# Optimization experiments

Measured on AMD Instinct MI355X. Metric: run time of the kernel, lower is better.

Reference implementation:

```python
import jax, jax.numpy as jnp
import numpy as np

NPOINT, RADIUS, NSAMPLE = 1024, 0.2, 32
EPS = 1e-5


def _fps(xyz, npoint):
    # Iterative farthest point sampling (deterministic start at index 0).
    B, N, _ = xyz.shape
    def step(carry, _):
        distance, farthest = carry
        centroid = jnp.take_along_axis(xyz, farthest[:, None, None], axis=1)  # (B,1,3)
        d = jnp.sum((xyz - centroid) ** 2, -1)                                # (B,N)
        distance = jnp.minimum(distance, d)
        return (distance, jnp.argmax(distance, -1)), farthest
    init = (jnp.full((B, N), 1e10, xyz.dtype), jnp.zeros((B,), jnp.int32))
    _, idx = jax.lax.scan(step, init, None, length=npoint)
    return idx.T  # (B, npoint)


def _gather(points, idx):
    # points (B,N,C), idx (B,S,K) -> (B,S,K,C)
    B, S, K = idx.shape
    flat = jnp.take_along_axis(points, idx.reshape(B, S * K)[:, :, None], axis=1)
    return flat.reshape(B, S, K, points.shape[-1])


def _query_ball(xyz, new_xyz):
    # For each centroid, first NSAMPLE point indices within RADIUS (pad with first hit).
    B, N, _ = xyz.shape
    sqr = jnp.sum((new_xyz[:, :, None, :] - xyz[:, None, :, :]) ** 2, -1)  # (B,S,N)
    gi = jnp.where(sqr > RADIUS ** 2, N, jnp.arange(N, dtype=jnp.int32)[None, None, :])
    gi = jnp.sort(gi, axis=-1)[:, :, :NSAMPLE]
    return jnp.where(gi == N, gi[:, :, :1], gi)  # (B,S,K)


def _cond_layer(x, t_embed, wt, bt, wc, bc, g, b):
    # ConditionalConv1d: x += time_mlp(gelu(t)); 1x1 conv; BatchNorm (batch stats); GELU.
    tp = jax.nn.gelu(t_embed, approximate=False) @ wt.T + bt      # (B,Cin)
    x = x + tp[:, None, None, :]
    y = jnp.einsum('bskc,oc->bsko', x, wc) + bc                   # (B,S,K,Cout)
    mu = jnp.mean(y, axis=(0, 1, 2))
    var = jnp.var(y, axis=(0, 1, 2))
    y = (y - mu) * jax.lax.rsqrt(var + EPS) * g + b
    return jax.nn.gelu(y, approximate=False)


def _forward(xyz, points, t_embed, params):
    fps_idx = _fps(xyz, NPOINT)                                        # (B,S)
    new_xyz = jnp.take_along_axis(xyz, fps_idx[:, :, None], axis=1)    # (B,S,3)
    idx = _query_ball(xyz, new_xyz)                                    # (B,S,K)
    grouped_xyz = _gather(xyz, idx) - new_xyz[:, :, None, :]           # (B,S,K,3)
    grouped_pts = _gather(jnp.swapaxes(points, 1, 2), idx)             # (B,S,K,C)
    x = jnp.concatenate([grouped_xyz, grouped_pts], -1)                # (B,S,K,C+3)
    for p in params:
        x = _cond_layer(x, t_embed, *p)
    new_points = jnp.swapaxes(jnp.max(x, axis=2), 1, 2)                # (B,Cout,S)
    return new_xyz, new_points


def setup_inputs() -> dict:
    key = jax.random.key(0)
    ks = iter(jax.random.split(key, 32))
    B, N, CIN, T = 8, 4096, 64, 128
    chans = [(CIN + 3, 64), (64, 64), (64, 128)]
    inp = {
        "xyz": jax.random.normal(next(ks), (B, N, 3), jnp.float32),
        "points": jax.random.normal(next(ks), (B, CIN, N), jnp.float32),
        "t_embed": jax.random.normal(next(ks), (B, T), jnp.float32),
    }
    for i, (ci, co) in enumerate(chans):
        inp[f"wt{i}"] = jax.random.normal(next(ks), (ci, T), jnp.float32) * 0.05
        inp[f"bt{i}"] = jnp.zeros((ci,), jnp.float32)
        inp[f"wc{i}"] = jax.random.normal(next(ks), (co, ci), jnp.float32) * 0.1
        inp[f"bc{i}"] = jnp.zeros((co,), jnp.float32)
        inp[f"g{i}"] = jnp.ones((co,), jnp.float32)
        inp[f"be{i}"] = jnp.zeros((co,), jnp.float32)
    return inp


def reference(xyz, points, t_embed,
              wt0, bt0, wc0, bc0, g0, be0,
              wt1, bt1, wc1, bc1, g1, be1,
              wt2, bt2, wc2, bc2, g2, be2):
    params = [(wt0, bt0, wc0, bc0, g0, be0),
              (wt1, bt1, wc1, bc1, g1, be1),
              (wt2, bt2, wc2, bc2, g2, be2)]
    return _forward(xyz, points, t_embed, params)
```

## Files before the change

kernel.cpp:

```cpp
#include <hip/hip_runtime.h>
#include <cmath>

#define Bc 8
#define Nc 4096
#define Sc 1024
#define Kc 32
#define Mc (Bc*Sc*Kc)

typedef float v2f __attribute__((ext_vector_type(2)));

__device__ __forceinline__ float gelu_f(float x){
  return 0.5f*x*(1.0f + erff(x*0.70710678f));
}

__device__ __forceinline__ v2f pk_add(v2f a, v2f b){
  v2f d; asm("v_pk_add_f32 %0, %1, %2" : "=v"(d) : "v"(a), "v"(b)); return d;
}
__device__ __forceinline__ v2f pk_mul(v2f a, v2f b){
  v2f d; asm("v_pk_mul_f32 %0, %1, %2" : "=v"(d) : "v"(a), "v"(b)); return d;
}

#define ROR_MAXF(v, n) { int _t = __builtin_amdgcn_update_dpp(__float_as_int(v), __float_as_int(v), 0x120|(n), 0xF, 0xF, false); \
                         v = fmaxf(v, __int_as_float(_t)); }
#define BC15_MAXF(v)   { int _t = __builtin_amdgcn_update_dpp(__float_as_int(v), __float_as_int(v), 0x142, 0xA, 0xF, false); \
                         v = fmaxf(v, __int_as_float(_t)); }
#define BC31_MAXF(v)   { int _t = __builtin_amdgcn_update_dpp(__float_as_int(v), __float_as_int(v), 0x143, 0xC, 0xF, false); \
                         v = fmaxf(v, __int_as_float(_t)); }

#define TK(v_, i_) { const bool _t = ((v_) > Bv) || (((v_) == Bv) && ((i_) < Bi)); \
  Bv = _t ? (v_) : Bv; Bi = _t ? (i_) : Bi; }

__global__ __launch_bounds__(256) void fused_front_kernel(
    const float* __restrict__ xyz, float* __restrict__ new_xyz,
    const float* __restrict__ points, float* __restrict__ pointsT,
    const float* __restrict__ t_embed,
    const float* __restrict__ wt0, const float* __restrict__ bt0,
    const float* __restrict__ wt1, const float* __restrict__ bt1,
    const float* __restrict__ wt2, const float* __restrict__ bt2,
    float* __restrict__ tp)
{
  __shared__ __align__(16) float smem[17424];
  const int bid = blockIdx.x;
  const int tid = threadIdx.x;

  if (bid < 8){
    const int b = bid;
    const int lane = tid & 63;
    const int wv = tid >> 6;
    const float* xb = xyz + b*Nc*3;
    float*    skv   = smem;
    unsigned* ski   = (unsigned*)(smem + 8);
    int*      shist = (int*)(smem + 16);
    float4*   c4    = (float4*)(smem + 1040);

    const int base = tid << 4;
    float4 f[12];
    const float4* src = (const float4*)(xb + base*3);
#pragma unroll
    for (int q=0;q<12;++q) f[q] = src[q];
#define AR(i) ((i)%4==0 ? f[(i)/4].x : (i)%4==1 ? f[(i)/4].y : (i)%4==2 ? f[(i)/4].z : f[(i)/4].w)
    v2f px2[8], py2[8], pz2[8], d2[8];
#pragma unroll
    for (int k=0;k<8;++k){
      px2[k].x = AR(6*k+0); py2[k].x = AR(6*k+1); pz2[k].x = AR(6*k+2);
      px2[k].y = AR(6*k+3); py2[k].y = AR(6*k+4); pz2[k].y = AR(6*k+5);
      c4[base+2*k  ] = make_float4(px2[k].x, py2[k].x, pz2[k].x, 0.f);
      c4[base+2*k+1] = make_float4(px2[k].y, py2[k].y, pz2[k].y, 0.f);
      d2[k].x = 1e10f; d2[k].y = 1e10f;
    }
#undef AR
    __syncthreads();
    int widx = 0;
    for (int it=0; it<Sc; ++it){
      const float4 cc = c4[widx];
      if (tid==0) shist[it] = widx;
      v2f ncx, ncy, ncz;
      ncx.x=-cc.x; ncx.y=-cc.x; ncy.x=-cc.y; ncy.y=-cc.y; ncz.x=-cc.z; ncz.y=-cc.z;
      float bvx=-1.0f, bvy=-1.0f;
#pragma unroll
      for (int k=0;k<8;++k){
        const v2f dx = pk_add(px2[k], ncx);
        const v2f dy = pk_add(py2[k], ncy);
        const v2f dz = pk_add(pz2[k], ncz);
        const v2f dd = pk_add(pk_add(pk_mul(dx,dx), pk_mul(dy,dy)), pk_mul(dz,dz));
        v2f dn;
        dn.x = fminf(d2[k].x, dd.x);
        dn.y = fminf(d2[k].y, dd.y);
        d2[k] = dn;
        bvx = fmaxf(bvx, dn.x);
        bvy = fmaxf(bvy, dn.y);
      }
      const float bv = fmaxf(bvx, bvy);
      unsigned bi_local = 0xFFFFFFFFu;
#pragma unroll
      for (int k=0;k<8;++k){
        const unsigned c0 = (d2[k].x == bv) ? (unsigned)(base + 2*k    ) : 0xFFFFFFFFu;
        const unsigned c1 = (d2[k].y == bv) ? (unsigned)(base + 2*k + 1) : 0xFFFFFFFFu;
        const unsigned cm = (c0 < c1) ? c0 : c1;
        bi_local = (cm < bi_local) ? cm : bi_local;
      }
      float mv = bv;
      ROR_MAXF(mv,1); ROR_MAXF(mv,2); ROR_MAXF(mv,4); ROR_MAXF(mv,8);
      BC15_MAXF(mv); BC31_MAXF(mv);
      mv = __int_as_float(__builtin_amdgcn_readlane(__float_as_int(mv), 63));
      const unsigned long long mk = __ballot(bv == mv);
      const int src_lane = __ffsll(mk) - 1;
      const unsigned bi = (unsigned)__builtin_amdgcn_readlane((int)bi_local, src_lane);
      const int p4 = (it & 1) << 2;
      if (lane==0){ skv[p4+wv] = mv; ski[p4+wv] = bi; }
      __syncthreads();
      const float4 m4 = *reinterpret_cast<const float4*>(&skv[p4]);
      const uint4  i4 = *reinterpret_cast<const uint4*>(&ski[p4]);
      float Bv = m4.x; unsigned Bi = i4.x;
      TK(m4.y, i4.y) TK(m4.z, i4.z) TK(m4.w, i4.w)
      widx = (int)Bi;
    }
    __syncthreads();
    for (int i = tid; i < Sc; i += 256){
      const float4 cc = c4[shist[i]];
      float* o = new_xyz + ((size_t)b*Sc + i)*3;
      o[0]=cc.x; o[1]=cc.y; o[2]=cc.z;
    }
  } else if (bid < 520){
    const int t  = bid - 8;
    const int tb = t >> 6;
    const int n0 = (t & 63) << 6;
    float (*tile)[65] = (float(*)[65])smem;
    const int sub = tid >> 6;
    const int ln  = tid & 63;
#pragma unroll 4
    for (int cp=0; cp<16; ++cp){
      const int c = (cp<<2) + sub;
      tile[c][ln] = points[((size_t)(tb*64+c))*Nc + n0 + ln];
    }
    __syncthreads();
#pragma unroll 4
    for (int np=0; np<16; ++np){
      const int nl = (np<<2) + sub;
      pointsT[((size_t)(tb*Nc + n0 + nl))*64 + ln] = tile[ln][nl];
    }
  } else {
    float* ge = smem;
    for (int i = tid; i < Bc*128; i += 256) ge[i] = gelu_f(t_embed[i]);
    __syncthreads();
    for (int i = tid; i < 3*Bc*68; i += 256){
      const int l = i / (Bc*68);
      const int r = i - l*(Bc*68);
      const int b = r / 68;
      const int c = r - b*68;
      const int ci = (l==0) ? 67 : 64;
      float v = 0.0f;
      if (c < ci){
        const float* wt = (l==0)?wt0:((l==1)?wt1:wt2);
        const float* bt = (l==0)?bt0:((l==1)?bt1:bt2);
        const float* w = wt + c*128;
        const float* g = ge + b*128;
        float acc = 0.0f;
        for (int t2=0;t2<128;++t2) acc = fmaf(g[t2], w[t2], acc);
        v = acc + bt[c];
      }
      tp[i] = v;
    }
  }
}

__global__ __launch_bounds__(256) void ball_kernel(const float* __restrict__ xyz,
    const float* __restrict__ new_xyz, int* __restrict__ ballidx){
  const int g = (blockIdx.x<<2) + (threadIdx.x>>6);
  const int lane = threadIdx.x & 63;
  const int w = threadIdx.x >> 6;
  const int b = g >> 10;
  const float* xb = xyz + b*Nc*3;
  const float cx = new_xyz[g*3+0];
  const float cy = new_xyz[g*3+1];
  const float cz = new_xyz[g*3+2];
  __shared__ int sidx[4][32];
  int total = 0;
  for (int base=0; base<Nc; base+=64){
    const int i = base + lane;
    float dx=__fsub_rn(cx, xb[i*3+0]);
    float dy=__fsub_rn(cy, xb[i*3+1]);
    float dz=__fsub_rn(cz, xb[i*3+2]);
    float sq=__fadd_rn(__fadd_rn(__fmul_rn(dx,dx),__fmul_rn(dy,dy)),__fmul_rn(dz,dz));
    bool hit = !(sq > 0.04f);
    unsigned long long m = __ballot(hit);
    if (hit){
      int pos = total + (int)__popcll(m & ((1ull<<lane)-1ull));
      if (pos < 32) sidx[w][pos] = i;
    }
    total += (int)__popcll(m);
    if (total >= 32) break;
  }
  __syncthreads();
  const int fill = (total < 32) ? total : 32;
  const int first = sidx[w][0];
  if (lane >= fill && lane < 32) sidx[w][lane] = first;
  if (lane < 32) ballidx[(g<<5)+lane] = sidx[w][lane];
}

__global__ __launch_bounds__(256) void gather_kernel(const float* __restrict__ xyz,
    const float* __restrict__ new_xyz, const float* __restrict__ pointsT,
    const int* __restrict__ ballidx, float* __restrict__ X){
  const int bs = blockIdx.x;
  const int b = bs >> 10;
  const int w = threadIdx.x >> 6;
  const int lane = threadIdx.x & 63;
  const float cx=new_xyz[bs*3+0], cy=new_xyz[bs*3+1], cz=new_xyz[bs*3+2];
  for (int k=w; k<32; k+=4){
    const int pidx = ballidx[(bs<<5)+k];
    const float* pt = pointsT + ((size_t)((b<<12)+pidx))*64;
    const float* xp = xyz + ((size_t)((b<<12)+pidx))*3;
    float* xr = X + (size_t)((bs<<5)+k)*68;
    float v;
    if      (lane==0) v = __fsub_rn(xp[0], cx);
    else if (lane==1) v = __fsub_rn(xp[1], cy);
    else if (lane==2) v = __fsub_rn(xp[2], cz);
    else              v = pt[lane-3];
    xr[lane] = v;
    if (lane < 4){
      int c = 64 + lane;
      xr[c] = (c<67) ? pt[c-3] : 0.0f;
    }
  }
}

template<int NORMIN, int CI_REAL, int CI_PAD, int LDX>
__global__ __launch_bounds__(256) void mm_kernel(const float* X,
    const float* __restrict__ wc, const float* __restrict__ tp,
    const float* __restrict__ sc_in, const float* __restrict__ sh_in,
    float* Y, float* __restrict__ pS, float* __restrict__ pQ, int o_base)
{
  __shared__ __align__(16) float wT[CI_PAD][64];
  __shared__ __align__(16) float tpr[CI_PAD];
  __shared__ __align__(16) float scN[64], shN[64];
  __shared__ float redS[4][64];
  __shared__ float redQ[4][64];
  const int tid = threadIdx.x;
  const int m0 = blockIdx.x << 8;
  const int b  = blockIdx.x >> 7;
  for (int idx = tid; idx < CI_PAD*64; idx += 256){
    int c = idx >> 6, o = idx & 63;
    wT[c][o] = (c < CI_REAL) ? wc[(o_base + o)*CI_REAL + c] : 0.0f;
  }
  if (tid < CI_PAD) tpr[tid] = tp[b*68 + tid];
  if (NORMIN && tid < 64){ scN[tid] = sc_in[tid]; shN[tid] = sh_in[tid]; }
  __syncthreads();
  const int rg = tid >> 2, cg = tid & 3;
  const float* x0 = X + (size_t)(m0 + (rg<<2)) * LDX;
  float4 acc[4][4];
#pragma unroll
  for (int r=0;r<4;++r)
#pragma unroll
    for (int q=0;q<4;++q) acc[r][q] = make_float4(0.f,0.f,0.f,0.f);

  for (int c = 0; c < CI_PAD; c += 4){
    const float4 tpv = *reinterpret_cast<const float4*>(&tpr[c]);
    float4 sci, shi;
    if (NORMIN){
      sci = *reinterpret_cast<const float4*>(&scN[c]);
      shi = *reinterpret_cast<const float4*>(&shN[c]);
    }
    float4 xr[4];
#pragma unroll
    for (int r=0;r<4;++r){
      float4 xv = *reinterpret_cast<const float4*>(x0 + r*LDX + c);
      if (NORMIN){
        xv.x = gelu_f(fmaf(xv.x, sci.x, shi.x));
        xv.y = gelu_f(fmaf(xv.y, sci.y, shi.y));
        xv.z = gelu_f(fmaf(xv.z, sci.z, shi.z));
        xv.w = gelu_f(fmaf(xv.w, sci.w, shi.w));
      }
      xr[r] = make_float4(xv.x+tpv.x, xv.y+tpv.y, xv.z+tpv.z, xv.w+tpv.w);
    }
#pragma unroll
    for (int cc=0; cc<4; ++cc){
      const float* wrow = &wT[c+cc][cg<<4];
      const float4 w0 = *reinterpret_cast<const float4*>(wrow);
      const float4 w1 = *reinterpret_cast<const float4*>(wrow+4);
      const float4 w2 = *reinterpret_cast<const float4*>(wrow+8);
      const float4 w3 = *reinterpret_cast<const float4*>(wrow+12);
#pragma unroll
      for (int r=0;r<4;++r){
        const float xs = (cc==0)?xr[r].x:((cc==1)?xr[r].y:((cc==2)?xr[r].z:xr[r].w));
        acc[r][0].x = fmaf(xs, w0.x, acc[r][0].x);
        acc[r][0].y = fmaf(xs, w0.y, acc[r][0].y);
        acc[r][0].z = fmaf(xs, w0.z, acc[r][0].z);
        acc[r][0].w = fmaf(xs, w0.w, acc[r][0].w);
        acc[r][1].x = fmaf(xs, w1.x, acc[r][1].x);
        acc[r][1].y = fmaf(xs, w1.y, acc[r][1].y);
        acc[r][1].z = fmaf(xs, w1.z, acc[r][1].z);
        acc[r][1].w = fmaf(xs, w1.w, acc[r][1].w);
        acc[r][2].x = fmaf(xs, w2.x, acc[r][2].x);
        acc[r][2].y = fmaf(xs, w2.y, acc[r][2].y);
        acc[r][2].z = fmaf(xs, w2.z, acc[r][2].z);
        acc[r][2].w = fmaf(xs, w2.w, acc[r][2].w);
        acc[r][3].x = fmaf(xs, w3.x, acc[r][3].x);
        acc[r][3].y = fmaf(xs, w3.y, acc[r][3].y);
        acc[r][3].z = fmaf(xs, w3.z, acc[r][3].z);
        acc[r][3].w = fmaf(xs, w3.w, acc[r][3].w);
      }
    }
  }
#pragma unroll
  for (int r=0;r<4;++r){
    float4* yp = reinterpret_cast<float4*>(Y + (size_t)(m0 + (rg<<2) + r)*64 + (cg<<4));
#pragma unroll
    for (int q=0;q<4;++q) yp[q] = acc[r][q];
  }
  float4 s[4], q2[4];
#pragma unroll
  for (int q=0;q<4;++q){
    float sx=0,sy=0,sz=0,sw=0, qx=0,qy=0,qz=0,qw=0;
#pragma unroll
    for (int r=0;r<4;++r){
      sx+=acc[r][q].x; qx+=acc[r][q].x*acc[r][q].x;
      sy+=acc[r][q].y; qy+=acc[r][q].y*acc[r][q].y;
      sz+=acc[r][q].z; qz+=acc[r][q].z*acc[r][q].z;
      sw+=acc[r][q].w; qw+=acc[r][q].w*acc[r][q].w;
    }
    s[q]=make_float4(sx,sy,sz,sw); q2[q]=make_float4(qx,qy,qz,qw);
  }
  const int lane = tid & 63, wvv = tid >> 6;
#pragma unroll
  for (int off=32; off>=4; off>>=1){
#pragma unroll
    for (int q=0;q<4;++q){
      s[q].x  += __shfl_down(s[q].x,  off);
      s[q].y  += __shfl_down(s[q].y,  off);
      s[q].z  += __shfl_down(s[q].z,  off);
      s[q].w  += __shfl_down(s[q].w,  off);
      q2[q].x += __shfl_down(q2[q].x, off);
      q2[q].y += __shfl_down(q2[q].y, off);
      q2[q].z += __shfl_down(q2[q].z, off);
      q2[q].w += __shfl_down(q2[q].w, off);
    }
  }
  if (lane < 4){
#pragma unroll
    for (int q=0;q<4;++q){
      redS[wvv][lane*16 + q*4 + 0] = s[q].x;
      redS[wvv][lane*16 + q*4 + 1] = s[q].y;
      redS[wvv][lane*16 + q*4 + 2] = s[q].z;
      redS[wvv][lane*16 + q*4 + 3] = s[q].w;
      redQ[wvv][lane*16 + q*4 + 0] = q2[q].x;
      redQ[wvv][lane*16 + q*4 + 1] = q2[q].y;
      redQ[wvv][lane*16 + q*4 + 2] = q2[q].z;
      redQ[wvv][lane*16 + q*4 + 3] = q2[q].w;
    }
  }
  __syncthreads();
  if (tid < 64){
    float a=0.f, bb=0.f;
#pragma unroll
    for (int w2=0; w2<4; ++w2){ a += redS[w2][tid]; bb += redQ[w2][tid]; }
    pS[(blockIdx.x<<6) + tid] = a;
    pQ[(blockIdx.x<<6) + tid] = bb;
  }
}

__global__ __launch_bounds__(256) void finalize_kernel(const float* __restrict__ pS,
    const float* __restrict__ pQ, const float* __restrict__ g, const float* __restrict__ be,
    float* __restrict__ scale, float* __restrict__ shift, int nblk){
  __shared__ float rS[4][64], rQ[4][64];
  const int o = threadIdx.x & 63;
  const int ch = threadIdx.x >> 6;
  const int per = nblk >> 2;
  float s=0.f, q=0.f;
  const int i0 = ch*per;
#pragma unroll 4
  for (int i=0;i<per;++i){
    s += pS[((i0+i)<<6)+o];
    q += pQ[((i0+i)<<6)+o];
  }
  rS[ch][o]=s; rQ[ch][o]=q;
  __syncthreads();
  if (threadIdx.x < 64){
    float ss = rS[0][o]+rS[1][o]+rS[2][o]+rS[3][o];
    float qq = rQ[0][o]+rQ[1][o]+rQ[2][o]+rQ[3][o];
    const float inv_n = 1.0f/(float)Mc;
    const float mu = ss*inv_n;
    const float var = qq*inv_n - mu*mu;
    const float rs = 1.0f/sqrtf(var + 1e-5f);
    const float sc = rs*g[o];
    scale[o] = sc;
    shift[o] = fmaf(-mu, sc, be[o]);
  }
}

__global__ __launch_bounds__(256) void pool_kernel(const float* __restrict__ Y,
    const float* __restrict__ scale, const float* __restrict__ shift,
    float* __restrict__ out, int o_base){
  __shared__ float pool[32][65];
  const int tid = threadIdx.x;
  const int b  = blockIdx.x >> 5;
  const int s0 = (blockIdx.x & 31) << 5;
  const int c  = tid & 63;
  const int sl0 = tid >> 6;
  const float sc = scale[c], sh = shift[c];
  for (int sp=0; sp<8; ++sp){
    const int sl = (sp<<2) + sl0;
    const int s = s0 + sl;
    const float* yp = Y + ((size_t)((b<<10)+s)<<5)*64 + c;
    float mx = -1e30f;
#pragma unroll 4
    for (int k=0;k<32;++k){
      float v = yp[(size_t)(k<<6)];
      v = gelu_f(fmaf(v, sc, sh));
      mx = fmaxf(mx, v);
    }
    pool[sl][c] = mx;
  }
  __syncthreads();
  for (int p=0;p<8;++p){
    const int c2 = (p<<3) + (tid>>5);
    const int sl = tid & 31;
    out[((size_t)((b<<7) + o_base + c2)<<10) + s0 + sl] = pool[sl][c2];
  }
}

extern "C" void kernel_launch(void* const* d_in, const int* in_sizes, int n_in,
                              void* d_out, int out_size, void* d_ws, size_t ws_size,
                              hipStream_t stream){
  const float* xyz     = (const float*)d_in[0];
  const float* points  = (const float*)d_in[1];
  const float* t_embed = (const float*)d_in[2];
  const float* wt0=(const float*)d_in[3],  *bt0=(const float*)d_in[4],  *wc0=(const float*)d_in[5];
  const float* g0 =(const float*)d_in[7],  *be0=(const float*)d_in[8];
  const float* wt1=(const float*)d_in[9],  *bt1=(const float*)d_in[10], *wc1=(const float*)d_in[11];
  const float* g1 =(const float*)d_in[13], *be1=(const float*)d_in[14];
  const float* wt2=(const float*)d_in[15], *bt2=(const float*)d_in[16], *wc2=(const float*)d_in[17];
  const float* g2 =(const float*)d_in[19], *be2=(const float*)d_in[20];

  float* out_xyz = (float*)d_out;
  float* out_pts = (float*)d_out + Bc*Sc*3;

  float* ws       = (float*)d_ws;
  float* tp       = ws + 0;
  float* pointsT  = ws + 2048;
  int*   ballidx  = (int*)(ws + 2099200);
  float* X        = ws + 2361344;
  float* Ya       = ws + 20187136;
  float* pS0      = ws + 36964352;
  float* pQ0      = ws + 37029888;
  float* pS1      = ws + 37095424;
  float* pQ1      = ws + 37160960;
  float* sc0      = ws + 37226496;
  float* sh0      = sc0 + 64;
  float* sc1      = sc0 + 128;
  float* sh1      = sc0 + 192;
  float* sc2      = sc0 + 256;
  float* sh2      = sc0 + 320;
  float* sc3      = sc0 + 384;
  float* sh3      = sc0 + 448;
  float* Yx       = X;

  fused_front_kernel<<<521, 256, 0, stream>>>(xyz, out_xyz, points, pointsT,
      t_embed, wt0,bt0, wt1,bt1, wt2,bt2, tp);
  ball_kernel<<<(Bc*Sc)/4, 256, 0, stream>>>(xyz, out_xyz, ballidx);
  gather_kernel<<<Bc*Sc, 256, 0, stream>>>(xyz, out_xyz, pointsT, ballidx, X);

  mm_kernel<0,67,68,68><<<Mc/256, 256, 0, stream>>>(X, wc0, tp, nullptr, nullptr, Ya, pS0, pQ0, 0);
  finalize_kernel<<<1, 256, 0, stream>>>(pS0, pQ0, g0, be0, sc0, sh0, Mc/256);

  mm_kernel<1,64,64,64><<<Mc/256, 256, 0, stream>>>(Ya, wc1, tp + 544, sc0, sh0, Ya, pS0, pQ0, 0);
  finalize_kernel<<<1, 256, 0, stream>>>(pS0, pQ0, g1, be1, sc1, sh1, Mc/256);

  mm_kernel<1,64,64,64><<<Mc/256, 256, 0, stream>>>(Ya, wc2, tp + 1088, sc1, sh1, Yx, pS0, pQ0, 0);
  mm_kernel<1,64,64,64><<<Mc/256, 256, 0, stream>>>(Ya, wc2, tp + 1088, sc1, sh1, Ya, pS1, pQ1, 64);
  finalize_kernel<<<1, 256, 0, stream>>>(pS0, pQ0, g2,    be2,    sc2, sh2, Mc/256);
  finalize_kernel<<<1, 256, 0, stream>>>(pS1, pQ1, g2+64, be2+64, sc3, sh3, Mc/256);

  pool_kernel<<<Bc*Sc/32, 256, 0, stream>>>(Yx, sc2, sh2, out_pts, 0);
  pool_kernel<<<Bc*Sc/32, 256, 0, stream>>>(Ya, sc3, sh3, out_pts, 64);
}
```

Measured before the change: 1.323 ms.

## Carry FPS centroid coords in registers and fuse ball query with gather

The FPS loop no longer stages all points in shared memory and looks up the selected centroid by index. Each lane now keeps the coordinates of its local argmax, broadcasts them via readlane, and reduces them through shared memory together with the value and index. Thread 0 writes new_xyz directly each iteration, replacing the final history pass. The ball query and gather kernels are merged so the 32 neighbor indices stay in shared memory instead of a global ballidx round trip. This saves a launch, but each wave now gathers its own 32 rows serially, and a __syncthreads was dropped in favour of wave-local shared memory access.

```diff
diff --git a/kernel.cpp b/kernel.cpp
--- a/kernel.cpp
+++ b/kernel.cpp
@@ -27,8 +27,8 @@
 #define BC31_MAXF(v)   { int _t = __builtin_amdgcn_update_dpp(__float_as_int(v), __float_as_int(v), 0x143, 0xC, 0xF, false); \
                          v = fmaxf(v, __int_as_float(_t)); }
 
-#define TK(v_, i_) { const bool _t = ((v_) > Bv) || (((v_) == Bv) && ((i_) < Bi)); \
-  Bv = _t ? (v_) : Bv; Bi = _t ? (i_) : Bi; }
+#define TK5(kk, i_) { const bool _t = ((kk).x > Bv) || (((kk).x == Bv) && ((i_) < Bi)); \
+  Bv=_t?(kk).x:Bv; Bi=_t?(i_):Bi; Bx=_t?(kk).y:Bx; By=_t?(kk).z:By; Bz=_t?(kk).w:Bz; }
 
 __global__ __launch_bounds__(256) void fused_front_kernel(
     const float* __restrict__ xyz, float* __restrict__ new_xyz,
@@ -39,7 +39,7 @@
     const float* __restrict__ wt2, const float* __restrict__ bt2,
     float* __restrict__ tp)
 {
-  __shared__ __align__(16) float smem[17424];
+  __shared__ __align__(16) float smem[4160];
   const int bid = blockIdx.x;
   const int tid = threadIdx.x;
 
@@ -48,10 +48,8 @@
     const int lane = tid & 63;
     const int wv = tid >> 6;
     const float* xb = xyz + b*Nc*3;
-    float*    skv   = smem;
-    unsigned* ski   = (unsigned*)(smem + 8);
-    int*      shist = (int*)(smem + 16);
-    float4*   c4    = (float4*)(smem + 1040);
+    float4*   skc = (float4*)smem;
+    unsigned* ski = (unsigned*)(smem + 32);
 
     const int base = tid << 4;
     float4 f[12];
@@ -64,18 +62,17 @@
     for (int k=0;k<8;++k){
       px2[k].x = AR(6*k+0); py2[k].x = AR(6*k+1); pz2[k].x = AR(6*k+2);
       px2[k].y = AR(6*k+3); py2[k].y = AR(6*k+4); pz2[k].y = AR(6*k+5);
-      c4[base+2*k  ] = make_float4(px2[k].x, py2[k].x, pz2[k].x, 0.f);
-      c4[base+2*k+1] = make_float4(px2[k].y, py2[k].y, pz2[k].y, 0.f);
       d2[k].x = 1e10f; d2[k].y = 1e10f;
     }
 #undef AR
-    __syncthreads();
-    int widx = 0;
+    float cx = xb[0], cy = xb[1], cz = xb[2];
     for (int it=0; it<Sc; ++it){
-      const float4 cc = c4[widx];
-      if (tid==0) shist[it] = widx;
+      if (tid==0){
+        float* o = new_xyz + ((size_t)b*Sc + it)*3;
+        o[0]=cx; o[1]=cy; o[2]=cz;
+      }
       v2f ncx, ncy, ncz;
-      ncx.x=-cc.x; ncx.y=-cc.x; ncy.x=-cc.y; ncy.y=-cc.y; ncz.x=-cc.z; ncz.y=-cc.z;
+      ncx.x=-cx; ncx.y=-cx; ncy.x=-cy; ncy.y=-cy; ncz.x=-cz; ncz.y=-cz;
       float bvx=-1.0f, bvy=-1.0f;
 #pragma unroll
       for (int k=0;k<8;++k){
@@ -91,35 +88,37 @@
         bvy = fmaxf(bvy, dn.y);
       }
       const float bv = fmaxf(bvx, bvy);
-      unsigned bi_local = 0xFFFFFFFFu;
+      unsigned bi = 0xFFFFFFFFu; float bx=0.f, by=0.f, bz=0.f;
 #pragma unroll
       for (int k=0;k<8;++k){
-        const unsigned c0 = (d2[k].x == bv) ? (unsigned)(base + 2*k    ) : 0xFFFFFFFFu;
-        const unsigned c1 = (d2[k].y == bv) ? (unsigned)(base + 2*k + 1) : 0xFFFFFFFFu;
-        const unsigned cm = (c0 < c1) ? c0 : c1;
-        bi_local = (cm < bi_local) ? cm : bi_local;
+        if ((d2[k].x == bv) && (bi == 0xFFFFFFFFu)){
+          bi = (unsigned)(base + 2*k); bx = px2[k].x; by = py2[k].x; bz = pz2[k].x;
+        }
+        if ((d2[k].y == bv) && (bi == 0xFFFFFFFFu)){
+          bi = (unsigned)(base + 2*k + 1); bx = px2[k].y; by = py2[k].y; bz = pz2[k].y;
+        }
       }
       float mv = bv;
       ROR_MAXF(mv,1); ROR_MAXF(mv,2); ROR_MAXF(mv,4); ROR_MAXF(mv,8);
       BC15_MAXF(mv); BC31_MAXF(mv);
       mv = __int_as_float(__builtin_amdgcn_readlane(__float_as_int(mv), 63));
       const unsigned long long mk = __ballot(bv == mv);
-      const int src_lane = __ffsll(mk) - 1;
-      const unsigned bi = (unsigned)__builtin_amdgcn_readlane((int)bi_local, src_lane);
+      const int sl = __ffsll(mk) - 1;
+      const unsigned wbi = (unsigned)__builtin_amdgcn_readlane((int)bi, sl);
+      const float wbx = __int_as_float(__builtin_amdgcn_readlane(__float_as_int(bx), sl));
+      const float wby = __int_as_float(__builtin_amdgcn_readlane(__float_as_int(by), sl));
+      const float wbz = __int_as_float(__builtin_amdgcn_readlane(__float_as_int(bz), sl));
       const int p4 = (it & 1) << 2;
-      if (lane==0){ skv[p4+wv] = mv; ski[p4+wv] = bi; }
+      if (lane==0){ skc[p4+wv] = make_float4(mv, wbx, wby, wbz); ski[p4+wv] = wbi; }
       __syncthreads();
-      const float4 m4 = *reinterpret_cast<const float4*>(&skv[p4]);
-      const uint4  i4 = *reinterpret_cast<const uint4*>(&ski[p4]);
-      float Bv = m4.x; unsigned Bi = i4.x;
-      TK(m4.y, i4.y) TK(m4.z, i4.z) TK(m4.w, i4.w)
-      widx = (int)Bi;
-    }
-    __syncthreads();
-    for (int i = tid; i < Sc; i += 256){
-      const float4 cc = c4[shist[i]];
-      float* o = new_xyz + ((size_t)b*Sc + i)*3;
-      o[0]=cc.x; o[1]=cc.y; o[2]=cc.z;
+      const float4 k0 = skc[p4+0];
+      const float4 k1 = skc[p4+1];
+      const float4 k2 = skc[p4+2];
+      const float4 k3 = skc[p4+3];
+      const uint4  ii = *reinterpret_cast<const uint4*>(&ski[p4]);
+      float Bv = k0.x; unsigned Bi = ii.x; float Bx = k0.y, By = k0.z, Bz = k0.w;
+      TK5(k1, ii.y) TK5(k2, ii.z) TK5(k3, ii.w)
+      cx = Bx; cy = By; cz = Bz;
     }
   } else if (bid < 520){
     const int t  = bid - 8;
@@ -164,8 +163,9 @@
   }
 }
 
-__global__ __launch_bounds__(256) void ball_kernel(const float* __restrict__ xyz,
-    const float* __restrict__ new_xyz, int* __restrict__ ballidx){
+__global__ __launch_bounds__(256) void ballgather_kernel(const float* __restrict__ xyz,
+    const float* __restrict__ new_xyz, const float* __restrict__ pointsT,
+    float* __restrict__ X){
   const int g = (blockIdx.x<<2) + (threadIdx.x>>6);
   const int lane = threadIdx.x & 63;
   const int w = threadIdx.x >> 6;
@@ -191,34 +191,21 @@
     total += (int)__popcll(m);
     if (total >= 32) break;
   }
-  __syncthreads();
   const int fill = (total < 32) ? total : 32;
   const int first = sidx[w][0];
   if (lane >= fill && lane < 32) sidx[w][lane] = first;
-  if (lane < 32) ballidx[(g<<5)+lane] = sidx[w][lane];
-}
-
-__global__ __launch_bounds__(256) void gather_kernel(const float* __restrict__ xyz,
-    const float* __restrict__ new_xyz, const float* __restrict__ pointsT,
-    const int* __restrict__ ballidx, float* __restrict__ X){
-  const int bs = blockIdx.x;
-  const int b = bs >> 10;
-  const int w = threadIdx.x >> 6;
-  const int lane = threadIdx.x & 63;
-  const float cx=new_xyz[bs*3+0], cy=new_xyz[bs*3+1], cz=new_xyz[bs*3+2];
-  for (int k=w; k<32; k+=4){
-    const int pidx = ballidx[(bs<<5)+k];
+  for (int k=0; k<32; ++k){
+    const int pidx = sidx[w][k];
     const float* pt = pointsT + ((size_t)((b<<12)+pidx))*64;
-    const float* xp = xyz + ((size_t)((b<<12)+pidx))*3;
-    float* xr = X + (size_t)((bs<<5)+k)*68;
+    float* xr = X + (size_t)((g<<5)+k)*68;
     float v;
-    if      (lane==0) v = __fsub_rn(xp[0], cx);
-    else if (lane==1) v = __fsub_rn(xp[1], cy);
-    else if (lane==2) v = __fsub_rn(xp[2], cz);
+    if      (lane==0) v = __fsub_rn(xb[pidx*3+0], cx);
+    else if (lane==1) v = __fsub_rn(xb[pidx*3+1], cy);
+    else if (lane==2) v = __fsub_rn(xb[pidx*3+2], cz);
     else              v = pt[lane-3];
     xr[lane] = v;
     if (lane < 4){
-      int c = 64 + lane;
+      const int c = 64 + lane;
       xr[c] = (c<67) ? pt[c-3] : 0.0f;
     }
   }
@@ -437,7 +424,6 @@
   float* ws       = (float*)d_ws;
   float* tp       = ws + 0;
   float* pointsT  = ws + 2048;
-  int*   ballidx  = (int*)(ws + 2099200);
   float* X        = ws + 2361344;
   float* Ya       = ws + 20187136;
   float* pS0      = ws + 36964352;
@@ -456,8 +442,7 @@
 
   fused_front_kernel<<<521, 256, 0, stream>>>(xyz, out_xyz, points, pointsT,
       t_embed, wt0,bt0, wt1,bt1, wt2,bt2, tp);
-  ball_kernel<<<(Bc*Sc)/4, 256, 0, stream>>>(xyz, out_xyz, ballidx);
-  gather_kernel<<<Bc*Sc, 256, 0, stream>>>(xyz, out_xyz, pointsT, ballidx, X);
+  ballgather_kernel<<<(Bc*Sc)/4, 256, 0, stream>>>(xyz, out_xyz, pointsT, X);
 
   mm_kernel<0,67,68,68><<<Mc/256, 256, 0, stream>>>(X, wc0, tp, nullptr, nullptr, Ya, pS0, pQ0, 0);
   finalize_kernel<<<1, 256, 0, stream>>>(pS0, pQ0, g0, be0, sc0, sh0, Mc/256);
```

Result: slower. 1.594 ms (+20.5%).

## Fuse ball query with gather and halve rows per thread in conv matmul

Applied to the files above, without the earlier changes.

The ball-query and gather kernels are merged, so each wave writes grouped xyz and point features straight from its shared-memory neighbour list. This drops the ballidx global round trip, one kernel launch and a block barrier. The 1x1-conv matmul kernel now computes 2 rows per thread instead of 4, with a register prefetch of the next input chunk, which doubles the number of blocks and lowers register pressure. The per-block partial-statistics buffers are moved and enlarged to hold the doubled block count. In exchange, each wave now gathers its 32 neighbours one after another, and each matmul block loads its weight tile for half as many rows.

```diff
diff --git a/kernel.cpp b/kernel.cpp
--- a/kernel.cpp
+++ b/kernel.cpp
@@ -164,8 +164,9 @@
   }
 }
 
-__global__ __launch_bounds__(256) void ball_kernel(const float* __restrict__ xyz,
-    const float* __restrict__ new_xyz, int* __restrict__ ballidx){
+__global__ __launch_bounds__(256) void ballgather_kernel(const float* __restrict__ xyz,
+    const float* __restrict__ new_xyz, const float* __restrict__ pointsT,
+    float* __restrict__ X){
   const int g = (blockIdx.x<<2) + (threadIdx.x>>6);
   const int lane = threadIdx.x & 63;
   const int w = threadIdx.x >> 6;
@@ -191,34 +192,21 @@
     total += (int)__popcll(m);
     if (total >= 32) break;
   }
-  __syncthreads();
   const int fill = (total < 32) ? total : 32;
   const int first = sidx[w][0];
   if (lane >= fill && lane < 32) sidx[w][lane] = first;
-  if (lane < 32) ballidx[(g<<5)+lane] = sidx[w][lane];
-}
-
-__global__ __launch_bounds__(256) void gather_kernel(const float* __restrict__ xyz,
-    const float* __restrict__ new_xyz, const float* __restrict__ pointsT,
-    const int* __restrict__ ballidx, float* __restrict__ X){
-  const int bs = blockIdx.x;
-  const int b = bs >> 10;
-  const int w = threadIdx.x >> 6;
-  const int lane = threadIdx.x & 63;
-  const float cx=new_xyz[bs*3+0], cy=new_xyz[bs*3+1], cz=new_xyz[bs*3+2];
-  for (int k=w; k<32; k+=4){
-    const int pidx = ballidx[(bs<<5)+k];
+  for (int k=0; k<32; ++k){
+    const int pidx = sidx[w][k];
     const float* pt = pointsT + ((size_t)((b<<12)+pidx))*64;
-    const float* xp = xyz + ((size_t)((b<<12)+pidx))*3;
-    float* xr = X + (size_t)((bs<<5)+k)*68;
+    float* xr = X + (size_t)((g<<5)+k)*68;
     float v;
-    if      (lane==0) v = __fsub_rn(xp[0], cx);
-    else if (lane==1) v = __fsub_rn(xp[1], cy);
-    else if (lane==2) v = __fsub_rn(xp[2], cz);
+    if      (lane==0) v = __fsub_rn(xb[pidx*3+0], cx);
+    else if (lane==1) v = __fsub_rn(xb[pidx*3+1], cy);
+    else if (lane==2) v = __fsub_rn(xb[pidx*3+2], cz);
     else              v = pt[lane-3];
     xr[lane] = v;
     if (lane < 4){
-      int c = 64 + lane;
+      const int c = 64 + lane;
       xr[c] = (c<67) ? pt[c-3] : 0.0f;
     }
   }
@@ -236,8 +224,8 @@
   __shared__ float redS[4][64];
   __shared__ float redQ[4][64];
   const int tid = threadIdx.x;
-  const int m0 = blockIdx.x << 8;
-  const int b  = blockIdx.x >> 7;
+  const int m0 = blockIdx.x << 7;
+  const int b  = blockIdx.x >> 8;
   for (int idx = tid; idx < CI_PAD*64; idx += 256){
     int c = idx >> 6, o = idx & 63;
     wT[c][o] = (c < CI_REAL) ? wc[(o_base + o)*CI_REAL + c] : 0.0f;
@@ -246,32 +234,38 @@
   if (NORMIN && tid < 64){ scN[tid] = sc_in[tid]; shN[tid] = sh_in[tid]; }
   __syncthreads();
   const int rg = tid >> 2, cg = tid & 3;
-  const float* x0 = X + (size_t)(m0 + (rg<<2)) * LDX;
-  float4 acc[4][4];
-#pragma unroll
-  for (int r=0;r<4;++r)
+  const float* x0 = X + (size_t)(m0 + (rg<<1)) * LDX;
+  float4 acc[2][4];
+#pragma unroll
+  for (int r=0;r<2;++r)
 #pragma unroll
     for (int q=0;q<4;++q) acc[r][q] = make_float4(0.f,0.f,0.f,0.f);
 
+  float4 xpf0 = *reinterpret_cast<const float4*>(x0);
+  float4 xpf1 = *reinterpret_cast<const float4*>(x0 + LDX);
+#pragma unroll
   for (int c = 0; c < CI_PAD; c += 4){
+    float4 xc0 = xpf0, xc1 = xpf1;
+    if (c + 4 < CI_PAD){
+      xpf0 = *reinterpret_cast<const float4*>(x0 + (c+4));
+      xpf1 = *reinterpret_cast<const float4*>(x0 + LDX + (c+4));
+    }
     const float4 tpv = *reinterpret_cast<const float4*>(&tpr[c]);
-    float4 sci, shi;
     if (NORMIN){
-      sci = *reinterpret_cast<const float4*>(&scN[c]);
-      shi = *reinterpret_cast<const float4*>(&shN[c]);
-    }
-    float4 xr[4];
-#pragma unroll
-    for (int r=0;r<4;++r){
-      float4 xv = *reinterpret_cast<const float4*>(x0 + r*LDX + c);
-      if (NORMIN){
-        xv.x = gelu_f(fmaf(xv.x, sci.x, shi.x));
-        xv.y = gelu_f(fmaf(xv.y, sci.y, shi.y));
-        xv.z = gelu_f(fmaf(xv.z, sci.z, shi.z));
-        xv.w = gelu_f(fmaf(xv.w, sci.w, shi.w));
-      }
-      xr[r] = make_float4(xv.x+tpv.x, xv.y+tpv.y, xv.z+tpv.z, xv.w+tpv.w);
-    }
+      const float4 sci = *reinterpret_cast<const float4*>(&scN[c]);
+      const float4 shi = *reinterpret_cast<const float4*>(&shN[c]);
+      xc0.x = gelu_f(fmaf(xc0.x, sci.x, shi.x));
+      xc0.y = gelu_f(fmaf(xc0.y, sci.y, shi.y));
+      xc0.z = gelu_f(fmaf(xc0.z, sci.z, shi.z));
+      xc0.w = gelu_f(fmaf(xc0.w, sci.w, shi.w));
+      xc1.x = gelu_f(fmaf(xc1.x, sci.x, shi.x));
+      xc1.y = gelu_f(fmaf(xc1.y, sci.y, shi.y));
+      xc1.z = gelu_f(fmaf(xc1.z, sci.z, shi.z));
+      xc1.w = gelu_f(fmaf(xc1.w, sci.w, shi.w));
+    }
+    float4 xr[2];
+    xr[0] = make_float4(xc0.x+tpv.x, xc0.y+tpv.y, xc0.z+tpv.z, xc0.w+tpv.w);
+    xr[1] = make_float4(xc1.x+tpv.x, xc1.y+tpv.y, xc1.z+tpv.z, xc1.w+tpv.w);
 #pragma unroll
     for (int cc=0; cc<4; ++cc){
       const float* wrow = &wT[c+cc][cg<<4];
@@ -280,7 +274,7 @@
       const float4 w2 = *reinterpret_cast<const float4*>(wrow+8);
       const float4 w3 = *reinterpret_cast<const float4*>(wrow+12);
 #pragma unroll
-      for (int r=0;r<4;++r){
+      for (int r=0;r<2;++r){
         const float xs = (cc==0)?xr[r].x:((cc==1)?xr[r].y:((cc==2)?xr[r].z:xr[r].w));
         acc[r][0].x = fmaf(xs, w0.x, acc[r][0].x);
         acc[r][0].y = fmaf(xs, w0.y, acc[r][0].y);
@@ -302,23 +296,20 @@
     }
   }
 #pragma unroll
-  for (int r=0;r<4;++r){
-    float4* yp = reinterpret_cast<float4*>(Y + (size_t)(m0 + (rg<<2) + r)*64 + (cg<<4));
+  for (int r=0;r<2;++r){
+    float4* yp = reinterpret_cast<float4*>(Y + (size_t)(m0 + (rg<<1) + r)*64 + (cg<<4));
 #pragma unroll
     for (int q=0;q<4;++q) yp[q] = acc[r][q];
   }
   float4 s[4], q2[4];
 #pragma unroll
   for (int q=0;q<4;++q){
-    float sx=0,sy=0,sz=0,sw=0, qx=0,qy=0,qz=0,qw=0;
-#pragma unroll
-    for (int r=0;r<4;++r){
-      sx+=acc[r][q].x; qx+=acc[r][q].x*acc[r][q].x;
-      sy+=acc[r][q].y; qy+=acc[r][q].y*acc[r][q].y;
-      sz+=acc[r][q].z; qz+=acc[r][q].z*acc[r][q].z;
-      sw+=acc[r][q].w; qw+=acc[r][q].w*acc[r][q].w;
-    }
-    s[q]=make_float4(sx,sy,sz,sw); q2[q]=make_float4(qx,qy,qz,qw);
+    s[q]  = make_float4(acc[0][q].x+acc[1][q].x, acc[0][q].y+acc[1][q].y,
+                        acc[0][q].z+acc[1][q].z, acc[0][q].w+acc[1][q].w);
+    q2[q] = make_float4(acc[0][q].x*acc[0][q].x + acc[1][q].x*acc[1][q].x,
+                        acc[0][q].y*acc[0][q].y + acc[1][q].y*acc[1][q].y,
+                        acc[0][q].z*acc[0][q].z + acc[1][q].z*acc[1][q].z,
+                        acc[0][q].w*acc[0][q].w + acc[1][q].w*acc[1][q].w);
   }
   const int lane = tid & 63, wvv = tid >> 6;
 #pragma unroll
@@ -437,13 +428,12 @@
   float* ws       = (float*)d_ws;
   float* tp       = ws + 0;
   float* pointsT  = ws + 2048;
-  int*   ballidx  = (int*)(ws + 2099200);
+  float* pS1      = ws + 2099200;
+  float* pQ1      = ws + 2230272;
   float* X        = ws + 2361344;
   float* Ya       = ws + 20187136;
   float* pS0      = ws + 36964352;
-  float* pQ0      = ws + 37029888;
-  float* pS1      = ws + 37095424;
-  float* pQ1      = ws + 37160960;
+  float* pQ0      = ws + 37095424;
   float* sc0      = ws + 37226496;
   float* sh0      = sc0 + 64;
   float* sc1      = sc0 + 128;
@@ -454,21 +444,22 @@
   float* sh3      = sc0 + 448;
   float* Yx       = X;
 
+  const int NBLK = Mc/128;
+
   fused_front_kernel<<<521, 256, 0, stream>>>(xyz, out_xyz, points, pointsT,
       t_embed, wt0,bt0, wt1,bt1, wt2,bt2, tp);
-  ball_kernel<<<(Bc*Sc)/4, 256, 0, stream>>>(xyz, out_xyz, ballidx);
-  gather_kernel<<<Bc*Sc, 256, 0, stream>>>(xyz, out_xyz, pointsT, ballidx, X);
-
-  mm_kernel<0,67,68,68><<<Mc/256, 256, 0, stream>>>(X, wc0, tp, nullptr, nullptr, Ya, pS0, pQ0, 0);
-  finalize_kernel<<<1, 256, 0, stream>>>(pS0, pQ0, g0, be0, sc0, sh0, Mc/256);
-
-  mm_kernel<1,64,64,64><<<Mc/256, 256, 0, stream>>>(Ya, wc1, tp + 544, sc0, sh0, Ya, pS0, pQ0, 0);
-  finalize_kernel<<<1, 256, 0, stream>>>(pS0, pQ0, g1, be1, sc1, sh1, Mc/256);
-
-  mm_kernel<1,64,64,64><<<Mc/256, 256, 0, stream>>>(Ya, wc2, tp + 1088, sc1, sh1, Yx, pS0, pQ0, 0);
-  mm_kernel<1,64,64,64><<<Mc/256, 256, 0, stream>>>(Ya, wc2, tp + 1088, sc1, sh1, Ya, pS1, pQ1, 64);
-  finalize_kernel<<<1, 256, 0, stream>>>(pS0, pQ0, g2,    be2,    sc2, sh2, Mc/256);
-  finalize_kernel<<<1, 256, 0, stream>>>(pS1, pQ1, g2+64, be2+64, sc3, sh3, Mc/256);
+  ballgather_kernel<<<(Bc*Sc)/4, 256, 0, stream>>>(xyz, out_xyz, pointsT, X);
+
+  mm_kernel<0,67,68,68><<<NBLK, 256, 0, stream>>>(X, wc0, tp, nullptr, nullptr, Ya, pS0, pQ0, 0);
+  finalize_kernel<<<1, 256, 0, stream>>>(pS0, pQ0, g0, be0, sc0, sh0, NBLK);
+
+  mm_kernel<1,64,64,64><<<NBLK, 256, 0, stream>>>(Ya, wc1, tp + 544, sc0, sh0, Ya, pS0, pQ0, 0);
+  finalize_kernel<<<1, 256, 0, stream>>>(pS0, pQ0, g1, be1, sc1, sh1, NBLK);
+
+  mm_kernel<1,64,64,64><<<NBLK, 256, 0, stream>>>(Ya, wc2, tp + 1088, sc1, sh1, Yx, pS0, pQ0, 0);
+  mm_kernel<1,64,64,64><<<NBLK, 256, 0, stream>>>(Ya, wc2, tp + 1088, sc1, sh1, Ya, pS1, pQ1, 64);
+  finalize_kernel<<<1, 256, 0, stream>>>(pS0, pQ0, g2,    be2,    sc2, sh2, NBLK);
+  finalize_kernel<<<1, 256, 0, stream>>>(pS1, pQ1, g2+64, be2+64, sc3, sh3, NBLK);
 
   pool_kernel<<<Bc*Sc/32, 256, 0, stream>>>(Yx, sc2, sh2, out_pts, 0);
   pool_kernel<<<Bc*Sc/32, 256, 0, stream>>>(Ya, sc3, sh3, out_pts, 64);
```

Result: slower. 5.248 ms (+296.6%).
